# Performance work log

Measured on AMD Instinct MI355X. Metric: run time of the kernel, lower is better.

The kernel has to match this reference:

```python
import jax, jax.numpy as jnp
import numpy as np

N = 50000      # num nodes
HID = 64       # hidden_dim
N2V = 64       # node2vec dim
E = 800000     # num edges
EP = 100000    # prediction edges
L = 2          # num_layers
EPS = 1e-5     # BatchNorm eps


def setup_inputs() -> dict:
    key = jax.random.key(0)
    ks = jax.random.split(key, 8)
    edge_index = jax.random.randint(ks[0], (2, E), 0, N)
    pred_edge = jax.random.randint(ks[1], (EP, 2), 0, N)
    id_emb = jax.random.normal(ks[2], (N, HID), jnp.float32) * 0.1      # learnable ID embedding
    n2v_emb = jax.random.normal(ks[3], (N, N2V), jnp.float32) * 0.1     # frozen node2vec embedding
    proj_w = jax.random.normal(ks[4], (HID + N2V, HID), jnp.float32) / np.sqrt(HID + N2V)
    proj_b = jnp.zeros((HID,), jnp.float32)
    conv_w = jax.random.normal(ks[5], (L, HID, HID), jnp.float32) / np.sqrt(HID)
    conv_b = jnp.zeros((L, HID), jnp.float32)
    bn_gamma = jnp.ones((L, HID), jnp.float32)
    bn_beta = jnp.zeros((L, HID), jnp.float32)
    return {"edge_index": edge_index, "pred_edge": pred_edge, "id_emb": id_emb,
            "n2v_emb": n2v_emb, "proj_w": proj_w, "proj_b": proj_b,
            "conv_w": conv_w, "conv_b": conv_b, "bn_gamma": bn_gamma, "bn_beta": bn_beta}


def reference(edge_index, pred_edge, id_emb, n2v_emb, proj_w, proj_b, conv_w, conv_b, bn_gamma, bn_beta):
    # input projection of concatenated embeddings: [N, HID+N2V] @ [HID+N2V, HID]
    x = jnp.concatenate([id_emb, n2v_emb], axis=1) @ proj_w + proj_b

    # GCN normalization with self-loops: norm_e = d^-1/2[src] * d^-1/2[dst]
    loops = jnp.arange(N, dtype=edge_index.dtype)
    row = jnp.concatenate([edge_index[0], loops])   # source nodes
    col = jnp.concatenate([edge_index[1], loops])   # destination nodes
    deg = jax.ops.segment_sum(jnp.ones(row.shape, x.dtype), col, num_segments=N)
    dis = jnp.where(deg > 0, jax.lax.rsqrt(deg), 0.0)
    norm = dis[row] * dis[col]                      # [E+N]

    for l in range(L):
        h = x @ conv_w[l]                                                    # [N, HID]
        agg = jax.ops.segment_sum(norm[:, None] * h[row], col, num_segments=N) + conv_b[l]
        # BatchNorm1d (training-mode batch stats over nodes)
        mu = agg.mean(axis=0)
        var = agg.var(axis=0)
        xn = (agg - mu) * jax.lax.rsqrt(var + EPS) * bn_gamma[l] + bn_beta[l]
        x = x + jax.nn.relu(xn)                                              # residual (shapes match)

    # dot-product link decoder
    z = x
    return (z[pred_edge[:, 0]] * z[pred_edge[:, 1]]).sum(axis=1)
```

## Files before the change

kernel.cpp:

```cpp
#include <hip/hip_runtime.h>

#define NN 50000
#define HID 64
#define NE 800000
#define NP 100000
#define BN_EPS 1e-5f
#define NB1 196

static inline size_t alignup(size_t x) { return (x + 255) & ~(size_t)255; }

__device__ __forceinline__ void f4fma(float a, const float4& w, float4& c) {
    c.x += a * w.x; c.y += a * w.y; c.z += a * w.z; c.w += a * w.w;
}
__device__ __forceinline__ void f4add(const float4& a, float4& c) {
    c.x += a.x; c.y += a.y; c.z += a.z; c.w += a.w;
}
__device__ __forceinline__ unsigned bfpack(float a, float b) {
    unsigned ua = __float_as_uint(a), ub = __float_as_uint(b);
    ua = (ua + 0x7fffu + ((ua >> 16) & 1u)) >> 16;
    ub = (ub + 0x7fffu + ((ub >> 16) & 1u)) >> 16;
    return ua | (ub << 16);
}
__device__ __forceinline__ float4 bf2f4(uint2 u) {
    float4 r;
    r.x = __uint_as_float(u.x << 16);
    r.y = __uint_as_float(u.x & 0xffff0000u);
    r.z = __uint_as_float(u.y << 16);
    r.w = __uint_as_float(u.y & 0xffff0000u);
    return r;
}


__global__ __launch_bounds__(256) void k_zero(int* __restrict__ cnt, float* __restrict__ sums,
                                              int* __restrict__ cursor) {
    int i = blockIdx.x * blockDim.x + threadIdx.x;
    if (i < NN) cnt[i] = 0;
    if (i < 256) sums[i] = 0.f;
    if (i == 0) *cursor = 0;
}


__global__ __launch_bounds__(256) void k_count(const int* __restrict__ col,
                                               int* __restrict__ cnt, int* __restrict__ rank) {
    int e = blockIdx.x * blockDim.x + threadIdx.x;
    if (e < NE) rank[e] = atomicAdd(&cnt[col[e]], 1);
}


__global__ __launch_bounds__(256) void k_alloc(const int* __restrict__ cnt,
                                               int* __restrict__ offs,
                                               float* __restrict__ dis,
                                               int* __restrict__ cursor) {
    __shared__ int s[256];
    __shared__ int base;
    int t = threadIdx.x;
    int i = blockIdx.x * 256 + t;
    int v = (i < NN) ? cnt[i] : 0;
    if (i < NN) dis[i] = rsqrtf((float)(v + 1));
    int va = (v + 7) & ~7;
    s[t] = va;
    __syncthreads();
    for (int off = 1; off < 256; off <<= 1) {
        int add = (t >= off) ? s[t - off] : 0;
        __syncthreads();
        s[t] += add;
        __syncthreads();
    }
    if (t == 255) base = atomicAdd(cursor, s[255]);
    __syncthreads();
    if (i < NN) offs[i] = base + s[t] - va;
}


__global__ __launch_bounds__(256) void k_fill(const int* __restrict__ row, const int* __restrict__ col,
                                              const int* __restrict__ rank, const int* __restrict__ offs,
                                              unsigned short* __restrict__ csr) {
    int e = blockIdx.x * blockDim.x + threadIdx.x;
    if (e >= NE) return;
    csr[offs[col[e]] + rank[e]] = (unsigned short)row[e];
}


__global__ __launch_bounds__(256) void k_proj(const float* __restrict__ id_emb,
                                              const float* __restrict__ n2v,
                                              const float* __restrict__ W,
                                              const float* __restrict__ b,
                                              const float* __restrict__ dis,
                                              float* __restrict__ x,
                                              unsigned short* __restrict__ xh) {
    __shared__ unsigned short Wlh[128 * 64];
    __shared__ unsigned short Al[32 * 132];
    int tid = threadIdx.x;
    int node0 = blockIdx.x * 32;
    const float2* W2f = (const float2*)W;
#pragma unroll
    for (int it = 0; it < 16; ++it) {
        int i = it * 256 + tid;
        float2 w = W2f[i];
        *(unsigned*)&Wlh[2 * i] = bfpack(w.x, w.y);
    }
    const float2* id2 = (const float2*)id_emb;
    const float2* nv2 = (const float2*)n2v;
#pragma unroll
    for (int it = 0; it < 8; ++it) {
        int i = it * 256 + tid;
        int r = i >> 6, kp = i & 63;
        int n = node0 + r;
        float2 v = make_float2(0.f, 0.f);
        if (n < NN) v = (kp < 32) ? id2[n * 32 + kp] : nv2[n * 32 + (kp - 32)];
        *(unsigned*)&Al[r * 132 + 2 * kp] = bfpack(v.x, v.y);
    }
    __syncthreads();
    int sub = tid >> 4, q = tid & 15;
    const uint2* W2 = (const uint2*)Wlh;
    float4* x4 = (float4*)x;
    uint2* xh2 = (uint2*)xh;
    float4 bb = ((const float4*)b)[q];
    float4 c0 = bb, c1 = bb;
#pragma unroll 4
    for (int k4 = 0; k4 < 32; ++k4) {
        float4 w0 = bf2f4(W2[(k4 * 4 + 0) * 16 + q]);
        float4 w1 = bf2f4(W2[(k4 * 4 + 1) * 16 + q]);
        float4 w2 = bf2f4(W2[(k4 * 4 + 2) * 16 + q]);
        float4 w3 = bf2f4(W2[(k4 * 4 + 3) * 16 + q]);
        float4 a0 = bf2f4(*(const uint2*)&Al[(sub * 2 + 0) * 132 + k4 * 4]);
        float4 a1 = bf2f4(*(const uint2*)&Al[(sub * 2 + 1) * 132 + k4 * 4]);
        f4fma(a0.x, w0, c0); f4fma(a0.y, w1, c0); f4fma(a0.z, w2, c0); f4fma(a0.w, w3, c0);
        f4fma(a1.x, w0, c1); f4fma(a1.y, w1, c1); f4fma(a1.z, w2, c1); f4fma(a1.w, w3, c1);
    }
    int n0 = node0 + sub * 2;
    if (n0 + 0 < NN) { float d = dis[n0+0]; x4[(n0+0)*16+q] = c0;
        xh2[(n0+0)*16+q] = make_uint2(bfpack(c0.x*d,c0.y*d), bfpack(c0.z*d,c0.w*d)); }
    if (n0 + 1 < NN) { float d = dis[n0+1]; x4[(n0+1)*16+q] = c1;
        xh2[(n0+1)*16+q] = make_uint2(bfpack(c1.x*d,c1.y*d), bfpack(c1.z*d,c1.w*d)); }
}


__global__ __launch_bounds__(256) void k_gather(const int* __restrict__ offs,
                                                const int* __restrict__ cnt,
                                                const unsigned short* __restrict__ csr,
                                                const float* __restrict__ dis,
                                                const unsigned short* __restrict__ xh,
                                                unsigned short* __restrict__ th) {
    int gw = (blockIdx.x * blockDim.x + threadIdx.x) >> 6;
    int lane = threadIdx.x & 63;
    int sub = lane >> 4, q = lane & 15;
    int node = gw * 4 + sub;
    if (node >= NN) return;
    const uint2* xh2 = (const uint2*)xh;
    float4 acc = make_float4(0.f, 0.f, 0.f, 0.f);
    const unsigned short* cs = csr + offs[node];
    int c = cnt[node];
    int jj = 0;
    for (; jj + 7 < c; jj += 8) {
        uint4 s8 = *(const uint4*)(cs + jj);
        int s0 = s8.x & 0xffff, s1 = s8.x >> 16;
        int s2 = s8.y & 0xffff, s3 = s8.y >> 16;
        int s4 = s8.z & 0xffff, s5 = s8.z >> 16;
        int s6 = s8.w & 0xffff, s7 = s8.w >> 16;
        uint2 u0 = xh2[s0 * 16 + q];
        uint2 u1 = xh2[s1 * 16 + q];
        uint2 u2 = xh2[s2 * 16 + q];
        uint2 u3 = xh2[s3 * 16 + q];
        uint2 u4 = xh2[s4 * 16 + q];
        uint2 u5 = xh2[s5 * 16 + q];
        uint2 u6 = xh2[s6 * 16 + q];
        uint2 u7 = xh2[s7 * 16 + q];
        f4add(bf2f4(u0), acc); f4add(bf2f4(u1), acc);
        f4add(bf2f4(u2), acc); f4add(bf2f4(u3), acc);
        f4add(bf2f4(u4), acc); f4add(bf2f4(u5), acc);
        f4add(bf2f4(u6), acc); f4add(bf2f4(u7), acc);
    }
    for (; jj < c; ++jj) {
        uint2 u0 = xh2[cs[jj] * 16 + q];
        f4add(bf2f4(u0), acc);
    }
    f4add(bf2f4(xh2[node * 16 + q]), acc);
    float di = dis[node];
    acc.x *= di; acc.y *= di; acc.z *= di; acc.w *= di;
    ((uint2*)th)[node * 16 + q] = make_uint2(bfpack(acc.x, acc.y), bfpack(acc.z, acc.w));
}


__global__ __launch_bounds__(256) void k_gemm_stats(const unsigned short* __restrict__ th,
                                                    const float* __restrict__ W,
                                                    unsigned short* __restrict__ agg,
                                                    float* __restrict__ sums) {
    __shared__ float Wl[64 * 64];
    __shared__ float ls0[16][64];
    __shared__ float ls1[16][64];
    int tid = threadIdx.x;
    for (int i = tid; i < 64 * 64; i += 256) Wl[i] = W[i];
    __syncthreads();
    int sub = tid >> 4, q = tid & 15;
    const uint2* t2 = (const uint2*)th;
    const float4* W4 = (const float4*)Wl;
    uint2* agg2 = (uint2*)agg;
    float4 s1 = make_float4(0.f, 0.f, 0.f, 0.f), s2 = s1;
    const int ngroups = (NN + 63) / 64;
    for (int g = blockIdx.x; g < ngroups; g += gridDim.x) {
        int n0 = g * 64 + sub * 4;
        int r0 = min(n0 + 0, NN - 1), r1 = min(n0 + 1, NN - 1);
        int r2 = min(n0 + 2, NN - 1), r3 = min(n0 + 3, NN - 1);
        float4 c0 = make_float4(0.f,0.f,0.f,0.f), c1 = c0, c2 = c0, c3 = c0;
#pragma unroll 4
        for (int k4 = 0; k4 < 16; ++k4) {
            float4 a0 = bf2f4(t2[r0 * 16 + k4]);
            float4 a1 = bf2f4(t2[r1 * 16 + k4]);
            float4 a2 = bf2f4(t2[r2 * 16 + k4]);
            float4 a3 = bf2f4(t2[r3 * 16 + k4]);
            float4 w0 = W4[(k4 * 4 + 0) * 16 + q];
            float4 w1 = W4[(k4 * 4 + 1) * 16 + q];
            float4 w2 = W4[(k4 * 4 + 2) * 16 + q];
            float4 w3 = W4[(k4 * 4 + 3) * 16 + q];
            f4fma(a0.x, w0, c0); f4fma(a0.y, w1, c0); f4fma(a0.z, w2, c0); f4fma(a0.w, w3, c0);
            f4fma(a1.x, w0, c1); f4fma(a1.y, w1, c1); f4fma(a1.z, w2, c1); f4fma(a1.w, w3, c1);
            f4fma(a2.x, w0, c2); f4fma(a2.y, w1, c2); f4fma(a2.z, w2, c2); f4fma(a2.w, w3, c2);
            f4fma(a3.x, w0, c3); f4fma(a3.y, w1, c3); f4fma(a3.z, w2, c3); f4fma(a3.w, w3, c3);
        }
        if (n0 + 0 < NN) { agg2[(n0 + 0) * 16 + q] = make_uint2(bfpack(c0.x, c0.y), bfpack(c0.z, c0.w));
            s1.x += c0.x; s1.y += c0.y; s1.z += c0.z; s1.w += c0.w;
            s2.x += c0.x*c0.x; s2.y += c0.y*c0.y; s2.z += c0.z*c0.z; s2.w += c0.w*c0.w; }
        if (n0 + 1 < NN) { agg2[(n0 + 1) * 16 + q] = make_uint2(bfpack(c1.x, c1.y), bfpack(c1.z, c1.w));
            s1.x += c1.x; s1.y += c1.y; s1.z += c1.z; s1.w += c1.w;
            s2.x += c1.x*c1.x; s2.y += c1.y*c1.y; s2.z += c1.z*c1.z; s2.w += c1.w*c1.w; }
        if (n0 + 2 < NN) { agg2[(n0 + 2) * 16 + q] = make_uint2(bfpack(c2.x, c2.y), bfpack(c2.z, c2.w));
            s1.x += c2.x; s1.y += c2.y; s1.z += c2.z; s1.w += c2.w;
            s2.x += c2.x*c2.x; s2.y += c2.y*c2.y; s2.z += c2.z*c2.z; s2.w += c2.w*c2.w; }
        if (n0 + 3 < NN) { agg2[(n0 + 3) * 16 + q] = make_uint2(bfpack(c3.x, c3.y), bfpack(c3.z, c3.w));
            s1.x += c3.x; s1.y += c3.y; s1.z += c3.z; s1.w += c3.w;
            s2.x += c3.x*c3.x; s2.y += c3.y*c3.y; s2.z += c3.z*c3.z; s2.w += c3.w*c3.w; }
    }
    ls0[sub][q * 4 + 0] = s1.x; ls0[sub][q * 4 + 1] = s1.y;
    ls0[sub][q * 4 + 2] = s1.z; ls0[sub][q * 4 + 3] = s1.w;
    ls1[sub][q * 4 + 0] = s2.x; ls1[sub][q * 4 + 1] = s2.y;
    ls1[sub][q * 4 + 2] = s2.z; ls1[sub][q * 4 + 3] = s2.w;
    __syncthreads();
    if (tid < 64) {
        float a = 0.f;
#pragma unroll
        for (int r = 0; r < 16; ++r) a += ls0[r][tid];
        atomicAdd(&sums[tid], a);
    } else if (tid < 128) {
        int c = tid - 64;
        float a = 0.f;
#pragma unroll
        for (int r = 0; r < 16; ++r) a += ls1[r][c];
        atomicAdd(&sums[64 + c], a);
    }
}


__global__ __launch_bounds__(256) void k_bnupdate(const unsigned short* __restrict__ agg,
                                                  const float* __restrict__ sums,
                                                  const float* __restrict__ gamma,
                                                  const float* __restrict__ beta,
                                                  const float* __restrict__ dis,
                                                  int prescale,
                                                  float* __restrict__ x,
                                                  unsigned short* __restrict__ xh) {
    int i = blockIdx.x * blockDim.x + threadIdx.x;
    if (i >= NN * 16) return;
    int f4 = i & 15;
    const float invn = 1.0f / (float)NN;
    float4 sm = ((const float4*)sums)[f4];
    float4 sq = ((const float4*)(sums + 64))[f4];
    float4 g = ((const float4*)gamma)[f4];
    float4 be = ((const float4*)beta)[f4];
    float4 a = bf2f4(((const uint2*)agg)[i]);
    float4 xv = ((const float4*)x)[i];
    float mu, var, rstd, xn;
    mu = sm.x * invn; var = sq.x * invn - mu * mu; rstd = rsqrtf(var + BN_EPS);
    xn = (a.x - mu) * rstd * g.x + be.x; xv.x += fmaxf(xn, 0.f);
    mu = sm.y * invn; var = sq.y * invn - mu * mu; rstd = rsqrtf(var + BN_EPS);
    xn = (a.y - mu) * rstd * g.y + be.y; xv.y += fmaxf(xn, 0.f);
    mu = sm.z * invn; var = sq.z * invn - mu * mu; rstd = rsqrtf(var + BN_EPS);
    xn = (a.z - mu) * rstd * g.z + be.z; xv.z += fmaxf(xn, 0.f);
    mu = sm.w * invn; var = sq.w * invn - mu * mu; rstd = rsqrtf(var + BN_EPS);
    xn = (a.w - mu) * rstd * g.w + be.w; xv.w += fmaxf(xn, 0.f);
    ((float4*)x)[i] = xv;
    float d = prescale ? dis[i >> 4] : 1.0f;
    ((uint2*)xh)[i] = make_uint2(bfpack(xv.x * d, xv.y * d), bfpack(xv.z * d, xv.w * d));
}


__global__ __launch_bounds__(256) void k_decode(const int* __restrict__ pred,
                                                const unsigned short* __restrict__ zh,
                                                float* __restrict__ out) {
    int gw = (blockIdx.x * blockDim.x + threadIdx.x) >> 6;
    int lane = threadIdx.x & 63;
    int sub = lane >> 4, q = lane & 15;
    int p = gw * 4 + sub;
    if (p >= NP) return;
    const uint2* z2 = (const uint2*)zh;
    int a = pred[2 * p], b = pred[2 * p + 1];
    float4 va = bf2f4(z2[a * 16 + q]);
    float4 vb = bf2f4(z2[b * 16 + q]);
    float v = va.x * vb.x + va.y * vb.y + va.z * vb.z + va.w * vb.w;
    v += __shfl_xor(v, 1);
    v += __shfl_xor(v, 2);
    v += __shfl_xor(v, 4);
    v += __shfl_xor(v, 8);
    if (q == 0) out[p] = v;
}

extern "C" void kernel_launch(void* const* d_in, const int* in_sizes, int n_in,
                              void* d_out, int out_size, void* d_ws, size_t ws_size,
                              hipStream_t stream) {
    const int* edge_index = (const int*)d_in[0];
    const int* pred       = (const int*)d_in[1];
    const float* id_emb   = (const float*)d_in[2];
    const float* n2v      = (const float*)d_in[3];
    const float* proj_w   = (const float*)d_in[4];
    const float* proj_b   = (const float*)d_in[5];
    const float* conv_w   = (const float*)d_in[6];
    const float* gamma    = (const float*)d_in[8];
    const float* beta     = (const float*)d_in[9];
    float* out = (float*)d_out;

    char* ws = (char*)d_ws;
    size_t off = 0;
    float* dis   = (float*)(ws + off); off += alignup(NN * 4);
    int* cnt     = (int*)(ws + off);   off += alignup(NN * 4);
    int* offs    = (int*)(ws + off);   off += alignup(NN * 4);
    int* rank    = (int*)(ws + off);   off += alignup((size_t)NE * 4);
    int* cursor  = (int*)(ws + off);   off += alignup(4);
    unsigned short* csr = (unsigned short*)(ws + off); off += alignup((size_t)(NE + NN * 8) * 2);
    float* x     = (float*)(ws + off); off += alignup((size_t)NN * 64 * 4);
    unsigned short* agg = (unsigned short*)(ws + off); off += alignup((size_t)NN * 64 * 2);
    unsigned short* xh = (unsigned short*)(ws + off); off += alignup((size_t)NN * 64 * 2);
    unsigned short* th = (unsigned short*)(ws + off); off += alignup((size_t)NN * 64 * 2);
    float* sums  = (float*)(ws + off);

    const int* row = edge_index;
    const int* col = edge_index + NE;

    k_zero<<<NB1, 256, 0, stream>>>(cnt, sums, cursor);
    k_count<<<(NE + 255) / 256, 256, 0, stream>>>(col, cnt, rank);
    k_alloc<<<NB1, 256, 0, stream>>>(cnt, offs, dis, cursor);
    k_fill<<<(NE + 255) / 256, 256, 0, stream>>>(row, col, rank, offs, csr);

    k_proj<<<(NN + 31) / 32, 256, 0, stream>>>(id_emb, n2v, proj_w, proj_b, dis, x, xh);

    for (int l = 0; l < 2; ++l) {
        k_gather<<<((NN + 3) / 4 * 64 + 255) / 256, 256, 0, stream>>>(offs, cnt, csr, dis, xh, th);
        k_gemm_stats<<<512, 256, 0, stream>>>(th, conv_w + l * 64 * 64, agg, sums + l * 128);
        k_bnupdate<<<(NN * 16 + 255) / 256, 256, 0, stream>>>(agg, sums + l * 128, gamma + l * 64,
                                                              beta + l * 64, dis, (l == 0) ? 1 : 0, x, xh);
    }

    k_decode<<<(NP / 4 * 64 + 255) / 256, 256, 0, stream>>>(pred, xh, out);
}
```

Measured before the change: 200.3 us.

## Fuse neighbor gather with per-layer GEMM and BN stats in one kernel

New measurement: 219.5 us. 1.1x slower.

```diff
diff --git a/kernel.cpp b/kernel.cpp
--- a/kernel.cpp
+++ b/kernel.cpp
@@ -136,117 +136,111 @@
 }
 
 
-__global__ __launch_bounds__(256) void k_gather(const int* __restrict__ offs,
-                                                const int* __restrict__ cnt,
-                                                const unsigned short* __restrict__ csr,
-                                                const float* __restrict__ dis,
-                                                const unsigned short* __restrict__ xh,
-                                                unsigned short* __restrict__ th) {
-    int gw = (blockIdx.x * blockDim.x + threadIdx.x) >> 6;
-    int lane = threadIdx.x & 63;
-    int sub = lane >> 4, q = lane & 15;
-    int node = gw * 4 + sub;
-    if (node >= NN) return;
-    const uint2* xh2 = (const uint2*)xh;
-    float4 acc = make_float4(0.f, 0.f, 0.f, 0.f);
-    const unsigned short* cs = csr + offs[node];
-    int c = cnt[node];
-    int jj = 0;
-    for (; jj + 7 < c; jj += 8) {
-        uint4 s8 = *(const uint4*)(cs + jj);
-        int s0 = s8.x & 0xffff, s1 = s8.x >> 16;
-        int s2 = s8.y & 0xffff, s3 = s8.y >> 16;
-        int s4 = s8.z & 0xffff, s5 = s8.z >> 16;
-        int s6 = s8.w & 0xffff, s7 = s8.w >> 16;
-        uint2 u0 = xh2[s0 * 16 + q];
-        uint2 u1 = xh2[s1 * 16 + q];
-        uint2 u2 = xh2[s2 * 16 + q];
-        uint2 u3 = xh2[s3 * 16 + q];
-        uint2 u4 = xh2[s4 * 16 + q];
-        uint2 u5 = xh2[s5 * 16 + q];
-        uint2 u6 = xh2[s6 * 16 + q];
-        uint2 u7 = xh2[s7 * 16 + q];
-        f4add(bf2f4(u0), acc); f4add(bf2f4(u1), acc);
-        f4add(bf2f4(u2), acc); f4add(bf2f4(u3), acc);
-        f4add(bf2f4(u4), acc); f4add(bf2f4(u5), acc);
-        f4add(bf2f4(u6), acc); f4add(bf2f4(u7), acc);
-    }
-    for (; jj < c; ++jj) {
-        uint2 u0 = xh2[cs[jj] * 16 + q];
-        f4add(bf2f4(u0), acc);
-    }
-    f4add(bf2f4(xh2[node * 16 + q]), acc);
-    float di = dis[node];
-    acc.x *= di; acc.y *= di; acc.z *= di; acc.w *= di;
-    ((uint2*)th)[node * 16 + q] = make_uint2(bfpack(acc.x, acc.y), bfpack(acc.z, acc.w));
-}
-
-
-__global__ __launch_bounds__(256) void k_gemm_stats(const unsigned short* __restrict__ th,
-                                                    const float* __restrict__ W,
-                                                    unsigned short* __restrict__ agg,
-                                                    float* __restrict__ sums) {
+__global__ __launch_bounds__(512, 6) void k_gg(const int* __restrict__ offs,
+                                               const int* __restrict__ cnt,
+                                               const unsigned short* __restrict__ csr,
+                                               const float* __restrict__ dis,
+                                               const unsigned short* __restrict__ xh,
+                                               const float* __restrict__ W,
+                                               unsigned short* __restrict__ agg,
+                                               float* __restrict__ sums) {
     __shared__ float Wl[64 * 64];
-    __shared__ float ls0[16][64];
-    __shared__ float ls1[16][64];
+    __shared__ unsigned short T[32 * 68];
+    __shared__ float ls0[8][64];
+    __shared__ float ls1[8][64];
     int tid = threadIdx.x;
-    for (int i = tid; i < 64 * 64; i += 256) Wl[i] = W[i];
-    __syncthreads();
-    int sub = tid >> 4, q = tid & 15;
-    const uint2* t2 = (const uint2*)th;
+    int node0 = blockIdx.x * 32;
+    for (int i = tid; i < 64 * 64; i += 512) Wl[i] = W[i];
+    {
+        int wave = tid >> 6, lane = tid & 63;
+        int sub = lane >> 4, q = lane & 15;
+        int nl = wave * 4 + sub;
+        int node = node0 + nl;
+        const uint2* xh2 = (const uint2*)xh;
+        float4 acc = make_float4(0.f, 0.f, 0.f, 0.f);
+        if (node < NN) {
+            const unsigned short* cs = csr + offs[node];
+            int c = cnt[node];
+            int jj = 0;
+            for (; jj + 7 < c; jj += 8) {
+                uint4 s8 = *(const uint4*)(cs + jj);
+                int s0 = s8.x & 0xffff, s1 = s8.x >> 16;
+                int s2 = s8.y & 0xffff, s3 = s8.y >> 16;
+                int s4 = s8.z & 0xffff, s5 = s8.z >> 16;
+                int s6 = s8.w & 0xffff, s7 = s8.w >> 16;
+                uint2 u0 = xh2[s0 * 16 + q];
+                uint2 u1 = xh2[s1 * 16 + q];
+                uint2 u2 = xh2[s2 * 16 + q];
+                uint2 u3 = xh2[s3 * 16 + q];
+                uint2 u4 = xh2[s4 * 16 + q];
+                uint2 u5 = xh2[s5 * 16 + q];
+                uint2 u6 = xh2[s6 * 16 + q];
+                uint2 u7 = xh2[s7 * 16 + q];
+                f4add(bf2f4(u0), acc); f4add(bf2f4(u1), acc);
+                f4add(bf2f4(u2), acc); f4add(bf2f4(u3), acc);
+                f4add(bf2f4(u4), acc); f4add(bf2f4(u5), acc);
+                f4add(bf2f4(u6), acc); f4add(bf2f4(u7), acc);
+            }
+            for (; jj < c; ++jj) {
+                uint2 u0 = xh2[cs[jj] * 16 + q];
+                f4add(bf2f4(u0), acc);
+            }
+            f4add(bf2f4(xh2[node * 16 + q]), acc);
+            float di = dis[node];
+            acc.x *= di; acc.y *= di; acc.z *= di; acc.w *= di;
+        }
+        ((uint2*)T)[nl * 17 + q] = make_uint2(bfpack(acc.x, acc.y), bfpack(acc.z, acc.w));
+    }
+    __syncthreads();
+    int r = tid >> 4, c = tid & 15;
+    int node = node0 + r;
+    const uint2* T2 = (const uint2*)T;
     const float4* W4 = (const float4*)Wl;
-    uint2* agg2 = (uint2*)agg;
-    float4 s1 = make_float4(0.f, 0.f, 0.f, 0.f), s2 = s1;
-    const int ngroups = (NN + 63) / 64;
-    for (int g = blockIdx.x; g < ngroups; g += gridDim.x) {
-        int n0 = g * 64 + sub * 4;
-        int r0 = min(n0 + 0, NN - 1), r1 = min(n0 + 1, NN - 1);
-        int r2 = min(n0 + 2, NN - 1), r3 = min(n0 + 3, NN - 1);
-        float4 c0 = make_float4(0.f,0.f,0.f,0.f), c1 = c0, c2 = c0, c3 = c0;
+    float4 c0 = make_float4(0.f, 0.f, 0.f, 0.f);
 #pragma unroll 4
-        for (int k4 = 0; k4 < 16; ++k4) {
-            float4 a0 = bf2f4(t2[r0 * 16 + k4]);
-            float4 a1 = bf2f4(t2[r1 * 16 + k4]);
-            float4 a2 = bf2f4(t2[r2 * 16 + k4]);
-            float4 a3 = bf2f4(t2[r3 * 16 + k4]);
-            float4 w0 = W4[(k4 * 4 + 0) * 16 + q];
-            float4 w1 = W4[(k4 * 4 + 1) * 16 + q];
-            float4 w2 = W4[(k4 * 4 + 2) * 16 + q];
-            float4 w3 = W4[(k4 * 4 + 3) * 16 + q];
-            f4fma(a0.x, w0, c0); f4fma(a0.y, w1, c0); f4fma(a0.z, w2, c0); f4fma(a0.w, w3, c0);
-            f4fma(a1.x, w0, c1); f4fma(a1.y, w1, c1); f4fma(a1.z, w2, c1); f4fma(a1.w, w3, c1);
-            f4fma(a2.x, w0, c2); f4fma(a2.y, w1, c2); f4fma(a2.z, w2, c2); f4fma(a2.w, w3, c2);
-            f4fma(a3.x, w0, c3); f4fma(a3.y, w1, c3); f4fma(a3.z, w2, c3); f4fma(a3.w, w3, c3);
-        }
-        if (n0 + 0 < NN) { agg2[(n0 + 0) * 16 + q] = make_uint2(bfpack(c0.x, c0.y), bfpack(c0.z, c0.w));
-            s1.x += c0.x; s1.y += c0.y; s1.z += c0.z; s1.w += c0.w;
-            s2.x += c0.x*c0.x; s2.y += c0.y*c0.y; s2.z += c0.z*c0.z; s2.w += c0.w*c0.w; }
-        if (n0 + 1 < NN) { agg2[(n0 + 1) * 16 + q] = make_uint2(bfpack(c1.x, c1.y), bfpack(c1.z, c1.w));
-            s1.x += c1.x; s1.y += c1.y; s1.z += c1.z; s1.w += c1.w;
-            s2.x += c1.x*c1.x; s2.y += c1.y*c1.y; s2.z += c1.z*c1.z; s2.w += c1.w*c1.w; }
-        if (n0 + 2 < NN) { agg2[(n0 + 2) * 16 + q] = make_uint2(bfpack(c2.x, c2.y), bfpack(c2.z, c2.w));
-            s1.x += c2.x; s1.y += c2.y; s1.z += c2.z; s1.w += c2.w;
-            s2.x += c2.x*c2.x; s2.y += c2.y*c2.y; s2.z += c2.z*c2.z; s2.w += c2.w*c2.w; }
-        if (n0 + 3 < NN) { agg2[(n0 + 3) * 16 + q] = make_uint2(bfpack(c3.x, c3.y), bfpack(c3.z, c3.w));
-            s1.x += c3.x; s1.y += c3.y; s1.z += c3.z; s1.w += c3.w;
-            s2.x += c3.x*c3.x; s2.y += c3.y*c3.y; s2.z += c3.z*c3.z; s2.w += c3.w*c3.w; }
-    }
-    ls0[sub][q * 4 + 0] = s1.x; ls0[sub][q * 4 + 1] = s1.y;
-    ls0[sub][q * 4 + 2] = s1.z; ls0[sub][q * 4 + 3] = s1.w;
-    ls1[sub][q * 4 + 0] = s2.x; ls1[sub][q * 4 + 1] = s2.y;
-    ls1[sub][q * 4 + 2] = s2.z; ls1[sub][q * 4 + 3] = s2.w;
+    for (int k4 = 0; k4 < 16; ++k4) {
+        float4 a = bf2f4(T2[r * 17 + k4]);
+        float4 w0 = W4[(k4 * 4 + 0) * 16 + c];
+        float4 w1 = W4[(k4 * 4 + 1) * 16 + c];
+        float4 w2 = W4[(k4 * 4 + 2) * 16 + c];
+        float4 w3 = W4[(k4 * 4 + 3) * 16 + c];
+        f4fma(a.x, w0, c0); f4fma(a.y, w1, c0); f4fma(a.z, w2, c0); f4fma(a.w, w3, c0);
+    }
+    float4 s1 = make_float4(0.f,0.f,0.f,0.f), s2 = s1;
+    if (node < NN) {
+        ((uint2*)agg)[node * 16 + c] = make_uint2(bfpack(c0.x, c0.y), bfpack(c0.z, c0.w));
+        s1 = c0;
+        s2 = make_float4(c0.x*c0.x, c0.y*c0.y, c0.z*c0.z, c0.w*c0.w);
+    }
+    s1.x += __shfl_xor(s1.x, 16); s1.y += __shfl_xor(s1.y, 16);
+    s1.z += __shfl_xor(s1.z, 16); s1.w += __shfl_xor(s1.w, 16);
+    s2.x += __shfl_xor(s2.x, 16); s2.y += __shfl_xor(s2.y, 16);
+    s2.z += __shfl_xor(s2.z, 16); s2.w += __shfl_xor(s2.w, 16);
+    s1.x += __shfl_xor(s1.x, 32); s1.y += __shfl_xor(s1.y, 32);
+    s1.z += __shfl_xor(s1.z, 32); s1.w += __shfl_xor(s1.w, 32);
+    s2.x += __shfl_xor(s2.x, 32); s2.y += __shfl_xor(s2.y, 32);
+    s2.z += __shfl_xor(s2.z, 32); s2.w += __shfl_xor(s2.w, 32);
+    int wave = tid >> 6, lane = tid & 63;
+    if (lane < 16) {
+        ls0[wave][lane * 4 + 0] = s1.x; ls0[wave][lane * 4 + 1] = s1.y;
+        ls0[wave][lane * 4 + 2] = s1.z; ls0[wave][lane * 4 + 3] = s1.w;
+    } else if (lane < 32) {
+        int cc = lane - 16;
+        ls1[wave][cc * 4 + 0] = s2.x; ls1[wave][cc * 4 + 1] = s2.y;
+        ls1[wave][cc * 4 + 2] = s2.z; ls1[wave][cc * 4 + 3] = s2.w;
+    }
     __syncthreads();
     if (tid < 64) {
         float a = 0.f;
 #pragma unroll
-        for (int r = 0; r < 16; ++r) a += ls0[r][tid];
+        for (int w = 0; w < 8; ++w) a += ls0[w][tid];
         atomicAdd(&sums[tid], a);
     } else if (tid < 128) {
-        int c = tid - 64;
+        int cc = tid - 64;
         float a = 0.f;
 #pragma unroll
-        for (int r = 0; r < 16; ++r) a += ls1[r][c];
-        atomicAdd(&sums[64 + c], a);
+        for (int w = 0; w < 8; ++w) a += ls1[w][cc];
+        atomicAdd(&sums[64 + cc], a);
     }
 }
 
@@ -329,7 +323,6 @@
     float* x     = (float*)(ws + off); off += alignup((size_t)NN * 64 * 4);
     unsigned short* agg = (unsigned short*)(ws + off); off += alignup((size_t)NN * 64 * 2);
     unsigned short* xh = (unsigned short*)(ws + off); off += alignup((size_t)NN * 64 * 2);
-    unsigned short* th = (unsigned short*)(ws + off); off += alignup((size_t)NN * 64 * 2);
     float* sums  = (float*)(ws + off);
 
     const int* row = edge_index;
@@ -343,8 +336,8 @@
     k_proj<<<(NN + 31) / 32, 256, 0, stream>>>(id_emb, n2v, proj_w, proj_b, dis, x, xh);
 
     for (int l = 0; l < 2; ++l) {
-        k_gather<<<((NN + 3) / 4 * 64 + 255) / 256, 256, 0, stream>>>(offs, cnt, csr, dis, xh, th);
-        k_gemm_stats<<<512, 256, 0, stream>>>(th, conv_w + l * 64 * 64, agg, sums + l * 128);
+        k_gg<<<(NN + 31) / 32, 512, 0, stream>>>(offs, cnt, csr, dis, xh,
+                                                 conv_w + l * 64 * 64, agg, sums + l * 128);
         k_bnupdate<<<(NN * 16 + 255) / 256, 256, 0, stream>>>(agg, sums + l * 128, gamma + l * 64,
                                                               beta + l * 64, dis, (l == 0) ? 1 : 0, x, xh);
     }
```
